# Performance work log

Measured on AMD Instinct MI355X. Metric: run time of the kernel, lower is better.

The kernel has to match this reference:

```python
import jax, jax.numpy as jnp
import numpy as np

H = 16
D = 64
EPS = 1e-6

def _phi(x):
    # elu_feature_map: elu(x) + 1
    return jax.nn.elu(x) + 1.0

def setup_inputs() -> dict:
    key = jax.random.key(0)
    k1, k2, k3, k4 = jax.random.split(key, 4)
    B, N = 4, 4096
    query = jax.random.normal(k1, (B, N, H * D), dtype=jnp.float32)
    key_t = jax.random.normal(k2, (B, N, H * D), dtype=jnp.float32)
    value = jax.random.normal(k3, (B, N, H * D), dtype=jnp.float32)
    W_out = jax.random.normal(k4, (D, H * D), dtype=jnp.float32) * (1.0 / np.sqrt(H * D))
    b_out = jnp.zeros((D,), dtype=jnp.float32)
    return {"query": query, "key": key_t, "value": value, "W_out": W_out, "b_out": b_out}

def reference(query, key, value, W_out, b_out):
    B, N, _ = query.shape
    # b n (h d) -> b h n d
    def split_heads(x):
        return x.reshape(B, N, H, D).transpose(0, 2, 1, 3)
    q = split_heads(query)
    k = split_heads(key)
    v = split_heads(value)
    Q = _phi(q)  # [B,H,N,D]
    K = _phi(k)
    # KV aggregation: O(N D^2)
    KV = jnp.einsum('bhnd,bhnm->bhdm', K, v)          # [B,H,D,D]
    Ksum = K.sum(axis=2)                               # [B,H,D]
    Z = 1.0 / (jnp.einsum('bhnd,bhd->bhn', Q, Ksum) + EPS)  # [B,H,N]
    out = jnp.einsum('bhnd,bhdm,bhn->bhnm', Q, KV, Z)  # [B,H,N,D]
    # b h n d -> b n h d -> (b*n, h*d)
    out = out.transpose(0, 2, 1, 3).reshape(B * N, H * D)
    return out @ W_out.T + b_out
```

## Files before the change

### kernel.cpp

```cpp
#include <hip/hip_runtime.h>

#define B_  4
#define N_  4096
#define H_  16
#define D_  64
#define BH_ 64
#define EPS_ 1e-6f

__device__ __forceinline__ float phi(float x) {
    return x > 0.0f ? x + 1.0f : __expf(x);
}

__global__ __launch_bounds__(256) void k_kvpart(const float* __restrict__ K,
                                                const float* __restrict__ V,
                                                float* __restrict__ kvpart,
                                                float* __restrict__ kspart) {
    const int bh = blockIdx.x;
    const int s  = blockIdx.y;
    const int S  = gridDim.y;
    const int b  = bh >> 4;
    const int h  = bh & 15;
    const int t  = threadIdx.x;

    __shared__ float Ks[64][68];
    __shared__ float Vs[64][68];

    float acc[4][4] = {{0.f}};
    float ksum[4]   = {0.f, 0.f, 0.f, 0.f};
    const int dbase = (t >> 4) * 4;
    const int mbase = (t & 15) * 4;

    const float4* Kf4 = (const float4*)K;
    const float4* Vf4 = (const float4*)V;

    const int rows   = N_ / S;
    const int chunks = rows / 64;

    for (int chunk = 0; chunk < chunks; ++chunk) {
        const int n0 = s * rows + chunk * 64;
        __syncthreads();
#pragma unroll
        for (int rep = 0; rep < 4; ++rep) {
            int idx = t + rep * 256;
            int row = idx >> 4, c4 = idx & 15;
            size_t g = (size_t)(b * N_ + n0 + row) * 256 + h * 16 + c4;
            float4 kv = Kf4[g];
            float4 vv = Vf4[g];
            Ks[row][c4 * 4 + 0] = phi(kv.x);
            Ks[row][c4 * 4 + 1] = phi(kv.y);
            Ks[row][c4 * 4 + 2] = phi(kv.z);
            Ks[row][c4 * 4 + 3] = phi(kv.w);
            *(float4*)&Vs[row][c4 * 4] = vv;
        }
        __syncthreads();
#pragma unroll 8
        for (int n = 0; n < 64; ++n) {
            float4 kd = *(const float4*)&Ks[n][dbase];
            float4 vm = *(const float4*)&Vs[n][mbase];
            float kda[4] = {kd.x, kd.y, kd.z, kd.w};
            float vma[4] = {vm.x, vm.y, vm.z, vm.w};
#pragma unroll
            for (int i = 0; i < 4; ++i) {
#pragma unroll
                for (int j = 0; j < 4; ++j) acc[i][j] += kda[i] * vma[j];
                ksum[i] += kda[i];
            }
        }
    }

    float4* kvp4 = (float4*)kvpart;
    const size_t base = (size_t)(bh * S + s) * 4096;
#pragma unroll
    for (int i = 0; i < 4; ++i) {
        float4 o = make_float4(acc[i][0], acc[i][1], acc[i][2], acc[i][3]);
        kvp4[(base + (size_t)(dbase + i) * 64 + mbase) / 4] = o;
    }
    if ((t & 15) == 0) {
#pragma unroll
        for (int i = 0; i < 4; ++i)
            kspart[(size_t)(bh * S + s) * 64 + dbase + i] = ksum[i];
    }
}

__global__ __launch_bounds__(256) void k_makeM(const float* __restrict__ kvpart,
                                               const float* __restrict__ kspart,
                                               const float* __restrict__ W,
                                               float* __restrict__ M,
                                               float* __restrict__ Ksum,
                                               int S) {
    const int bh = blockIdx.x;
    const int h  = bh & 15;
    const int t  = threadIdx.x;

    __shared__ float KVs[64][68];
    __shared__ float Ws[64][68];

    const float4* kv4 = (const float4*)kvpart;
    const float4* W4  = (const float4*)W;

    for (int idx = t; idx < 1024; idx += 256) {
        int row = idx >> 4, c4 = idx & 15;
        float4 r = make_float4(0.f, 0.f, 0.f, 0.f);
        for (int s = 0; s < S; ++s) {
            float4 a = kv4[(size_t)(bh * S + s) * 1024 + idx];
            r.x += a.x; r.y += a.y; r.z += a.z; r.w += a.w;
        }
        *(float4*)&KVs[row][c4 * 4] = r;
        *(float4*)&Ws[row][c4 * 4] = W4[(size_t)row * 256 + h * 16 + c4];
    }
    if (t < 64) {
        float ks = 0.f;
        for (int s = 0; s < S; ++s) ks += kspart[(size_t)(bh * S + s) * 64 + t];
        Ksum[(size_t)bh * 64 + t] = ks;
    }
    __syncthreads();

    const int dbase = (t >> 4) * 4, jbase = (t & 15) * 4;
    float acc[4][4] = {{0.f}};
#pragma unroll 4
    for (int m4 = 0; m4 < 16; ++m4) {
        float4 kvr[4], wr[4];
#pragma unroll
        for (int i = 0; i < 4; ++i) kvr[i] = *(const float4*)&KVs[dbase + i][m4 * 4];
#pragma unroll
        for (int j = 0; j < 4; ++j) wr[j] = *(const float4*)&Ws[jbase + j][m4 * 4];
#pragma unroll
        for (int i = 0; i < 4; ++i)
#pragma unroll
            for (int j = 0; j < 4; ++j)
                acc[i][j] += kvr[i].x * wr[j].x + kvr[i].y * wr[j].y +
                             kvr[i].z * wr[j].z + kvr[i].w * wr[j].w;
    }
    float4* M4 = (float4*)M;
#pragma unroll
    for (int i = 0; i < 4; ++i)
        M4[((size_t)bh * 4096 + (size_t)(dbase + i) * 64 + jbase) / 4] =
            make_float4(acc[i][0], acc[i][1], acc[i][2], acc[i][3]);
}

__global__ __launch_bounds__(256) void k_out(const float* __restrict__ Q,
                                             const float* __restrict__ M,
                                             const float* __restrict__ Ksum,
                                             float* __restrict__ outpart) {
    const int nc = blockIdx.x;
    const int b  = blockIdx.y;
    const int hs = blockIdx.z;
    const int HS = gridDim.z;
    const int hper = H_ / HS;
    const int n0 = nc * 64;
    const int t  = threadIdx.x;

    __shared__ float Ms[64][68];
    __shared__ float QsT[64][65];
    __shared__ float zp[4][64];
    __shared__ float Kss[64];

    const int ibase = (t >> 4) * 4, jbase = (t & 15) * 4;
    const int qtr = t >> 6, zrow = t & 63;
    float acc[4][4] = {{0.f}};

    const float4* Qf4 = (const float4*)Q;
    const float4* Mf4 = (const float4*)M;

    for (int hh = 0; hh < hper; ++hh) {
        const int h  = hs * hper + hh;
        const int bh = b * 16 + h;
        __syncthreads();
#pragma unroll
        for (int rep = 0; rep < 4; ++rep) {
            int idx = t + rep * 256;
            int row = idx >> 4, c4 = idx & 15;
            *(float4*)&Ms[row][c4 * 4] = Mf4[(size_t)bh * 1024 + idx];
            float4 qq = Qf4[(size_t)(b * N_ + n0 + row) * 256 + h * 16 + c4];
            QsT[c4 * 4 + 0][row] = phi(qq.x);
            QsT[c4 * 4 + 1][row] = phi(qq.y);
            QsT[c4 * 4 + 2][row] = phi(qq.z);
            QsT[c4 * 4 + 3][row] = phi(qq.w);
        }
        if (t < 64) Kss[t] = Ksum[(size_t)bh * 64 + t];
        __syncthreads();

        {
            float part = 0.f;
#pragma unroll
            for (int dd = 0; dd < 16; ++dd) {
                int d = qtr * 16 + dd;
                part += QsT[d][zrow] * Kss[d];
            }
            zp[qtr][zrow] = part;
        }
        __syncthreads();

        float sacc[4][4] = {{0.f}};
#pragma unroll 8
        for (int d = 0; d < 64; ++d) {
            float4 qi = *(const float4*)&QsT[d][ibase];
            float4 mj = *(const float4*)&Ms[d][jbase];
            float qa[4] = {qi.x, qi.y, qi.z, qi.w};
            float ma[4] = {mj.x, mj.y, mj.z, mj.w};
#pragma unroll
            for (int i = 0; i < 4; ++i)
#pragma unroll
                for (int j = 0; j < 4; ++j) sacc[i][j] += qa[i] * ma[j];
        }
#pragma unroll
        for (int i = 0; i < 4; ++i) {
            int r = ibase + i;
            float z = 1.0f / (zp[0][r] + zp[1][r] + zp[2][r] + zp[3][r] + EPS_);
#pragma unroll
            for (int j = 0; j < 4; ++j) acc[i][j] += z * sacc[i][j];
        }
    }

    float4* O4 = (float4*)outpart;
    const size_t slice = (size_t)hs * (B_ * N_ * 64);
#pragma unroll
    for (int i = 0; i < 4; ++i) {
        float4 o = make_float4(acc[i][0], acc[i][1], acc[i][2], acc[i][3]);
        O4[(slice + (size_t)(b * N_ + n0 + ibase + i) * 64 + jbase) / 4] = o;
    }
}

__global__ __launch_bounds__(256) void k_red(const float* __restrict__ outpart,
                                             const float* __restrict__ bout,
                                             float* __restrict__ out, int HS) {
    const int p = blockIdx.x * 256 + threadIdx.x;
    const float4* P4 = (const float4*)outpart;
    const float4* B4 = (const float4*)bout;
    float4 o = B4[p & 15];
    const int stride = B_ * N_ * 64 / 4;
    for (int hs = 0; hs < HS; ++hs) {
        float4 a = P4[(size_t)hs * stride + p];
        o.x += a.x; o.y += a.y; o.z += a.z; o.w += a.w;
    }
    ((float4*)out)[p] = o;
}

extern "C" void kernel_launch(void* const* d_in, const int* in_sizes, int n_in,
                              void* d_out, int out_size, void* d_ws, size_t ws_size,
                              hipStream_t stream) {
    const float* q  = (const float*)d_in[0];
    const float* k  = (const float*)d_in[1];
    const float* v  = (const float*)d_in[2];
    const float* W  = (const float*)d_in[3];
    const float* bo = (const float*)d_in[4];
    float* out = (float*)d_out;

    int S = 16, HS = 4;
    {
        size_t need = ((size_t)BH_ * 16 * 4096 + (size_t)BH_ * 16 * 64 +
                       (size_t)BH_ * 4096 + BH_ * 64 +
                       (size_t)4 * B_ * N_ * 64) * 4;
        if (ws_size < need) { S = 4; HS = 1; }
    }

    float* ws      = (float*)d_ws;
    float* kvpart  = ws;
    float* kspart  = kvpart + (size_t)BH_ * S * 4096;
    float* M       = kspart + (size_t)BH_ * S * 64;
    float* Ksum    = M + (size_t)BH_ * 4096;
    float* outpart = Ksum + (size_t)BH_ * 64;

    k_kvpart<<<dim3(BH_, S), 256, 0, stream>>>(k, v, kvpart, kspart);
    k_makeM<<<BH_, 256, 0, stream>>>(kvpart, kspart, W, M, Ksum, S);
    k_out<<<dim3(N_ / 64, B_, HS), 256, 0, stream>>>(q, M, Ksum, outpart);
    k_red<<<B_ * N_ * 64 / 4 / 256, 256, 0, stream>>>(outpart, bo, out, HS);
}
```

Baseline: 263.5 us.

## Use packed fp16 dot2 in KV and output kernels with larger tiles

Converts phi(K), V, phi(Q), the projected M and Ksum to packed fp16 pairs in shared memory and accumulates with v_dot2 (fp16 inputs, fp32 accumulation). k_kvpart now splits the row chunk across four waves with 8x8 register tiles, then reduces the partials through shared memory. k_out processes 128 rows per block and computes the normaliser inside the main loop, so the separate z pass and its barrier go away. Split counts become compile-time constants and the workspace-size fallback is removed. This costs input precision and raises register pressure.

```diff
diff --git a/kernel.cpp b/kernel.cpp
--- a/kernel.cpp
+++ b/kernel.cpp
@@ -5,10 +5,26 @@
 #define H_  16
 #define D_  64
 #define BH_ 64
+#define S_  8
+#define HS_ 4
 #define EPS_ 1e-6f
+
+typedef _Float16 h2  __attribute__((ext_vector_type(2)));
+typedef float    f4v __attribute__((ext_vector_type(4)));
+
+struct H2x4 { h2 e[4]; };
+
+__device__ __forceinline__ H2x4 ld_h2x4(const h2* p) {
+    f4v r = *(const f4v*)p;
+    return __builtin_bit_cast(H2x4, r);
+}
 
 __device__ __forceinline__ float phi(float x) {
     return x > 0.0f ? x + 1.0f : __expf(x);
+}
+
+__device__ __forceinline__ float fdot2(h2 a, h2 b, float c) {
+    return __builtin_amdgcn_fdot2(a, b, c, false);
 }
 
 __global__ __launch_bounds__(256) void k_kvpart(const float* __restrict__ K,
@@ -17,77 +33,139 @@
                                                 float* __restrict__ kspart) {
     const int bh = blockIdx.x;
     const int s  = blockIdx.y;
-    const int S  = gridDim.y;
     const int b  = bh >> 4;
     const int h  = bh & 15;
     const int t  = threadIdx.x;
-
-    __shared__ float Ks[64][68];
-    __shared__ float Vs[64][68];
-
-    float acc[4][4] = {{0.f}};
-    float ksum[4]   = {0.f, 0.f, 0.f, 0.f};
-    const int dbase = (t >> 4) * 4;
-    const int mbase = (t & 15) * 4;
+    const int w  = t >> 6;
+    const int lane = t & 63;
+
+    __shared__ __align__(16) float pool[2 * 64 * 68];
+    __shared__ float ksred[4][64];
+
+    h2* Kp = (h2*)pool;
+    h2* Vp = (h2*)(pool + 2176);
+
+    const int dbase = (lane >> 3) * 8;
+    const int mbase = (lane & 7) * 8;
+
+    float acc[8][8] = {{0.f}};
+    float ksum[8]   = {0.f};
+    h2 one2; one2.x = (_Float16)1.0f; one2.y = (_Float16)1.0f;
 
     const float4* Kf4 = (const float4*)K;
     const float4* Vf4 = (const float4*)V;
 
-    const int rows   = N_ / S;
-    const int chunks = rows / 64;
-
-    for (int chunk = 0; chunk < chunks; ++chunk) {
-        const int n0 = s * rows + chunk * 64;
+    for (int chunk = 0; chunk < (N_ / S_) / 64; ++chunk) {
+        const int n0 = s * (N_ / S_) + chunk * 64;
         __syncthreads();
 #pragma unroll
-        for (int rep = 0; rep < 4; ++rep) {
+        for (int rep = 0; rep < 2; ++rep) {
             int idx = t + rep * 256;
-            int row = idx >> 4, c4 = idx & 15;
-            size_t g = (size_t)(b * N_ + n0 + row) * 256 + h * 16 + c4;
-            float4 kv = Kf4[g];
-            float4 vv = Vf4[g];
-            Ks[row][c4 * 4 + 0] = phi(kv.x);
-            Ks[row][c4 * 4 + 1] = phi(kv.y);
-            Ks[row][c4 * 4 + 2] = phi(kv.z);
-            Ks[row][c4 * 4 + 3] = phi(kv.w);
-            *(float4*)&Vs[row][c4 * 4] = vv;
+            int rp = idx >> 4, c4 = idx & 15;
+            size_t g = (size_t)(b * N_ + n0 + 2 * rp) * 256 + h * 16 + c4;
+            float4 a = Kf4[g];
+            float4 c = Kf4[g + 256];
+            H2x4 o;
+            o.e[0].x = (_Float16)phi(a.x); o.e[0].y = (_Float16)phi(c.x);
+            o.e[1].x = (_Float16)phi(a.y); o.e[1].y = (_Float16)phi(c.y);
+            o.e[2].x = (_Float16)phi(a.z); o.e[2].y = (_Float16)phi(c.z);
+            o.e[3].x = (_Float16)phi(a.w); o.e[3].y = (_Float16)phi(c.w);
+            *(f4v*)&Kp[rp * 68 + c4 * 4] = __builtin_bit_cast(f4v, o);
+        }
+#pragma unroll
+        for (int rep = 0; rep < 2; ++rep) {
+            int idx = t + rep * 256;
+            int rp = idx >> 4, c4 = idx & 15;
+            size_t g = (size_t)(b * N_ + n0 + 2 * rp) * 256 + h * 16 + c4;
+            float4 a = Vf4[g];
+            float4 c = Vf4[g + 256];
+            H2x4 o;
+            o.e[0].x = (_Float16)a.x; o.e[0].y = (_Float16)c.x;
+            o.e[1].x = (_Float16)a.y; o.e[1].y = (_Float16)c.y;
+            o.e[2].x = (_Float16)a.z; o.e[2].y = (_Float16)c.z;
+            o.e[3].x = (_Float16)a.w; o.e[3].y = (_Float16)c.w;
+            *(f4v*)&Vp[rp * 68 + c4 * 4] = __builtin_bit_cast(f4v, o);
         }
         __syncthreads();
-#pragma unroll 8
-        for (int n = 0; n < 64; ++n) {
-            float4 kd = *(const float4*)&Ks[n][dbase];
-            float4 vm = *(const float4*)&Vs[n][mbase];
-            float kda[4] = {kd.x, kd.y, kd.z, kd.w};
-            float vma[4] = {vm.x, vm.y, vm.z, vm.w};
-#pragma unroll
-            for (int i = 0; i < 4; ++i) {
-#pragma unroll
-                for (int j = 0; j < 4; ++j) acc[i][j] += kda[i] * vma[j];
-                ksum[i] += kda[i];
+#pragma unroll
+        for (int cc = 0; cc < 8; ++cc) {
+            int c = w * 8 + cc;
+            H2x4 kd0 = ld_h2x4(&Kp[c * 68 + dbase]);
+            H2x4 kd1 = ld_h2x4(&Kp[c * 68 + dbase + 4]);
+            H2x4 vm0 = ld_h2x4(&Vp[c * 68 + mbase]);
+            H2x4 vm1 = ld_h2x4(&Vp[c * 68 + mbase + 4]);
+            h2 kd[8] = {kd0.e[0], kd0.e[1], kd0.e[2], kd0.e[3],
+                        kd1.e[0], kd1.e[1], kd1.e[2], kd1.e[3]};
+            h2 vm[8] = {vm0.e[0], vm0.e[1], vm0.e[2], vm0.e[3],
+                        vm1.e[0], vm1.e[1], vm1.e[2], vm1.e[3]};
+#pragma unroll
+            for (int i = 0; i < 8; ++i) {
+#pragma unroll
+                for (int j = 0; j < 8; ++j) acc[i][j] = fdot2(kd[i], vm[j], acc[i][j]);
+                ksum[i] = fdot2(kd[i], one2, ksum[i]);
             }
         }
     }
 
-    float4* kvp4 = (float4*)kvpart;
-    const size_t base = (size_t)(bh * S + s) * 4096;
-#pragma unroll
-    for (int i = 0; i < 4; ++i) {
-        float4 o = make_float4(acc[i][0], acc[i][1], acc[i][2], acc[i][3]);
-        kvp4[(base + (size_t)(dbase + i) * 64 + mbase) / 4] = o;
-    }
-    if ((t & 15) == 0) {
-#pragma unroll
-        for (int i = 0; i < 4; ++i)
-            kspart[(size_t)(bh * S + s) * 64 + dbase + i] = ksum[i];
-    }
+    if ((lane & 7) == 0) {
+#pragma unroll
+        for (int i = 0; i < 8; ++i) ksred[w][dbase + i] = ksum[i];
+    }
+    float* Red = pool;
+    __syncthreads();
+
+#define WRITE_T(slot)                                                          \
+    {   float* T = Red + (slot) * 64 * 68;                                     \
+        _Pragma("unroll")                                                      \
+        for (int i = 0; i < 8; ++i) {                                          \
+            f4v o0 = {acc[i][0], acc[i][1], acc[i][2], acc[i][3]};             \
+            f4v o1 = {acc[i][4], acc[i][5], acc[i][6], acc[i][7]};             \
+            *(f4v*)&T[(dbase + i) * 68 + mbase]     = o0;                      \
+            *(f4v*)&T[(dbase + i) * 68 + mbase + 4] = o1;                      \
+        } }
+#define ADD_T(slot)                                                            \
+    {   float* T = Red + (slot) * 64 * 68;                                     \
+        _Pragma("unroll")                                                      \
+        for (int i = 0; i < 8; ++i) {                                          \
+            f4v r0 = *(f4v*)&T[(dbase + i) * 68 + mbase];                      \
+            f4v r1 = *(f4v*)&T[(dbase + i) * 68 + mbase + 4];                  \
+            acc[i][0] += r0[0]; acc[i][1] += r0[1];                            \
+            acc[i][2] += r0[2]; acc[i][3] += r0[3];                            \
+            acc[i][4] += r1[0]; acc[i][5] += r1[1];                            \
+            acc[i][6] += r1[2]; acc[i][7] += r1[3];                            \
+        } }
+
+    if (w == 1) WRITE_T(0);
+    if (w == 3) WRITE_T(1);
+    __syncthreads();
+    if (w == 0) ADD_T(0);
+    if (w == 2) ADD_T(1);
+    __syncthreads();
+    if (w == 2) WRITE_T(0);
+    __syncthreads();
+    if (w == 0) {
+        ADD_T(0);
+        float4* kvp4 = (float4*)kvpart;
+        const size_t base = (size_t)(bh * S_ + s) * 4096;
+#pragma unroll
+        for (int i = 0; i < 8; ++i) {
+            float4 o0 = make_float4(acc[i][0], acc[i][1], acc[i][2], acc[i][3]);
+            float4 o1 = make_float4(acc[i][4], acc[i][5], acc[i][6], acc[i][7]);
+            kvp4[(base + (size_t)(dbase + i) * 64 + mbase) / 4]     = o0;
+            kvp4[(base + (size_t)(dbase + i) * 64 + mbase + 4) / 4] = o1;
+        }
+        float ks = ksred[0][lane] + ksred[1][lane] + ksred[2][lane] + ksred[3][lane];
+        kspart[(size_t)(bh * S_ + s) * 64 + lane] = ks;
+    }
+#undef WRITE_T
+#undef ADD_T
 }
 
 __global__ __launch_bounds__(256) void k_makeM(const float* __restrict__ kvpart,
                                                const float* __restrict__ kspart,
                                                const float* __restrict__ W,
-                                               float* __restrict__ M,
-                                               float* __restrict__ Ksum,
-                                               int S) {
+                                               float* __restrict__ Mh,
+                                               float* __restrict__ Ksum) {
     const int bh = blockIdx.x;
     const int h  = bh & 15;
     const int t  = threadIdx.x;
@@ -101,8 +179,8 @@
     for (int idx = t; idx < 1024; idx += 256) {
         int row = idx >> 4, c4 = idx & 15;
         float4 r = make_float4(0.f, 0.f, 0.f, 0.f);
-        for (int s = 0; s < S; ++s) {
-            float4 a = kv4[(size_t)(bh * S + s) * 1024 + idx];
+        for (int s = 0; s < S_; ++s) {
+            float4 a = kv4[(size_t)(bh * S_ + s) * 1024 + idx];
             r.x += a.x; r.y += a.y; r.z += a.z; r.w += a.w;
         }
         *(float4*)&KVs[row][c4 * 4] = r;
@@ -110,7 +188,7 @@
     }
     if (t < 64) {
         float ks = 0.f;
-        for (int s = 0; s < S; ++s) ks += kspart[(size_t)(bh * S + s) * 64 + t];
+        for (int s = 0; s < S_; ++s) ks += kspart[(size_t)(bh * S_ + s) * 64 + t];
         Ksum[(size_t)bh * 64 + t] = ks;
     }
     __syncthreads();
@@ -131,105 +209,112 @@
                 acc[i][j] += kvr[i].x * wr[j].x + kvr[i].y * wr[j].y +
                              kvr[i].z * wr[j].z + kvr[i].w * wr[j].w;
     }
-    float4* M4 = (float4*)M;
-#pragma unroll
-    for (int i = 0; i < 4; ++i)
-        M4[((size_t)bh * 4096 + (size_t)(dbase + i) * 64 + jbase) / 4] =
-            make_float4(acc[i][0], acc[i][1], acc[i][2], acc[i][3]);
+    f4v* M4 = (f4v*)Mh;
+#pragma unroll
+    for (int p = 0; p < 2; ++p) {
+        int c = (dbase >> 1) + p;
+        H2x4 o;
+#pragma unroll
+        for (int j = 0; j < 4; ++j) {
+            o.e[j].x = (_Float16)acc[2 * p][j];
+            o.e[j].y = (_Float16)acc[2 * p + 1][j];
+        }
+        M4[((size_t)bh * 2048 + c * 64 + jbase) / 4] = __builtin_bit_cast(f4v, o);
+    }
 }
 
 __global__ __launch_bounds__(256) void k_out(const float* __restrict__ Q,
-                                             const float* __restrict__ M,
+                                             const float* __restrict__ Mh,
                                              const float* __restrict__ Ksum,
                                              float* __restrict__ outpart) {
     const int nc = blockIdx.x;
     const int b  = blockIdx.y;
     const int hs = blockIdx.z;
-    const int HS = gridDim.z;
-    const int hper = H_ / HS;
-    const int n0 = nc * 64;
+    const int n0 = nc * 128;
     const int t  = threadIdx.x;
 
-    __shared__ float Ms[64][68];
-    __shared__ float QsT[64][65];
-    __shared__ float zp[4][64];
-    __shared__ float Kss[64];
-
-    const int ibase = (t >> 4) * 4, jbase = (t & 15) * 4;
-    const int qtr = t >> 6, zrow = t & 63;
-    float acc[4][4] = {{0.f}};
+    __shared__ __align__(16) h2 QpT[32][132];
+    __shared__ __align__(16) h2 Msp[32][68];
+    __shared__ h2 Kssh[32];
+
+    const int ibase = (t >> 4) * 8;
+    const int jbase = (t & 15) * 4;
+    float acc_out[8][4] = {{0.f}};
 
     const float4* Qf4 = (const float4*)Q;
-    const float4* Mf4 = (const float4*)M;
-
-    for (int hh = 0; hh < hper; ++hh) {
-        const int h  = hs * hper + hh;
+    const f4v*    M4  = (const f4v*)Mh;
+
+    for (int hh = 0; hh < 4; ++hh) {
+        const int h  = hs * 4 + hh;
         const int bh = b * 16 + h;
         __syncthreads();
 #pragma unroll
-        for (int rep = 0; rep < 4; ++rep) {
+        for (int rep = 0; rep < 8; ++rep) {
             int idx = t + rep * 256;
             int row = idx >> 4, c4 = idx & 15;
-            *(float4*)&Ms[row][c4 * 4] = Mf4[(size_t)bh * 1024 + idx];
             float4 qq = Qf4[(size_t)(b * N_ + n0 + row) * 256 + h * 16 + c4];
-            QsT[c4 * 4 + 0][row] = phi(qq.x);
-            QsT[c4 * 4 + 1][row] = phi(qq.y);
-            QsT[c4 * 4 + 2][row] = phi(qq.z);
-            QsT[c4 * 4 + 3][row] = phi(qq.w);
-        }
-        if (t < 64) Kss[t] = Ksum[(size_t)bh * 64 + t];
+            h2 p0; p0.x = (_Float16)phi(qq.x); p0.y = (_Float16)phi(qq.y);
+            h2 p1; p1.x = (_Float16)phi(qq.z); p1.y = (_Float16)phi(qq.w);
+            QpT[2 * c4][row]     = p0;
+            QpT[2 * c4 + 1][row] = p1;
+        }
+#pragma unroll
+        for (int rep = 0; rep < 2; ++rep) {
+            int i2 = t + rep * 256;
+            int c = i2 >> 4, j4 = (i2 & 15) * 4;
+            *(f4v*)&Msp[c][j4] = M4[(size_t)bh * 512 + i2];
+        }
+        if (t < 32) {
+            h2 ks; ks.x = (_Float16)Ksum[(size_t)bh * 64 + 2 * t];
+            ks.y = (_Float16)Ksum[(size_t)bh * 64 + 2 * t + 1];
+            Kssh[t] = ks;
+        }
         __syncthreads();
 
-        {
-            float part = 0.f;
-#pragma unroll
-            for (int dd = 0; dd < 16; ++dd) {
-                int d = qtr * 16 + dd;
-                part += QsT[d][zrow] * Kss[d];
+        float sacc[8][4] = {{0.f}};
+        float zacc[8]    = {0.f};
+#pragma unroll 4
+        for (int c = 0; c < 32; ++c) {
+            H2x4 qa = ld_h2x4(&QpT[c][ibase]);
+            H2x4 qb = ld_h2x4(&QpT[c][ibase + 4]);
+            H2x4 mm = ld_h2x4(&Msp[c][jbase]);
+            h2 ks = Kssh[c];
+            h2 q[8] = {qa.e[0], qa.e[1], qa.e[2], qa.e[3],
+                       qb.e[0], qb.e[1], qb.e[2], qb.e[3]};
+#pragma unroll
+            for (int i = 0; i < 8; ++i) {
+                zacc[i] = fdot2(q[i], ks, zacc[i]);
+#pragma unroll
+                for (int j = 0; j < 4; ++j) sacc[i][j] = fdot2(q[i], mm.e[j], sacc[i][j]);
             }
-            zp[qtr][zrow] = part;
-        }
-        __syncthreads();
-
-        float sacc[4][4] = {{0.f}};
-#pragma unroll 8
-        for (int d = 0; d < 64; ++d) {
-            float4 qi = *(const float4*)&QsT[d][ibase];
-            float4 mj = *(const float4*)&Ms[d][jbase];
-            float qa[4] = {qi.x, qi.y, qi.z, qi.w};
-            float ma[4] = {mj.x, mj.y, mj.z, mj.w};
-#pragma unroll
-            for (int i = 0; i < 4; ++i)
-#pragma unroll
-                for (int j = 0; j < 4; ++j) sacc[i][j] += qa[i] * ma[j];
-        }
-#pragma unroll
-        for (int i = 0; i < 4; ++i) {
-            int r = ibase + i;
-            float z = 1.0f / (zp[0][r] + zp[1][r] + zp[2][r] + zp[3][r] + EPS_);
-#pragma unroll
-            for (int j = 0; j < 4; ++j) acc[i][j] += z * sacc[i][j];
+        }
+#pragma unroll
+        for (int i = 0; i < 8; ++i) {
+            float z = 1.0f / (zacc[i] + EPS_);
+#pragma unroll
+            for (int j = 0; j < 4; ++j) acc_out[i][j] += z * sacc[i][j];
         }
     }
 
     float4* O4 = (float4*)outpart;
     const size_t slice = (size_t)hs * (B_ * N_ * 64);
 #pragma unroll
-    for (int i = 0; i < 4; ++i) {
-        float4 o = make_float4(acc[i][0], acc[i][1], acc[i][2], acc[i][3]);
+    for (int i = 0; i < 8; ++i) {
+        float4 o = make_float4(acc_out[i][0], acc_out[i][1], acc_out[i][2], acc_out[i][3]);
         O4[(slice + (size_t)(b * N_ + n0 + ibase + i) * 64 + jbase) / 4] = o;
     }
 }
 
 __global__ __launch_bounds__(256) void k_red(const float* __restrict__ outpart,
                                              const float* __restrict__ bout,
-                                             float* __restrict__ out, int HS) {
+                                             float* __restrict__ out) {
     const int p = blockIdx.x * 256 + threadIdx.x;
     const float4* P4 = (const float4*)outpart;
     const float4* B4 = (const float4*)bout;
     float4 o = B4[p & 15];
     const int stride = B_ * N_ * 64 / 4;
-    for (int hs = 0; hs < HS; ++hs) {
+#pragma unroll
+    for (int hs = 0; hs < HS_; ++hs) {
         float4 a = P4[(size_t)hs * stride + p];
         o.x += a.x; o.y += a.y; o.z += a.z; o.w += a.w;
     }
@@ -246,23 +331,15 @@
     const float* bo = (const float*)d_in[4];
     float* out = (float*)d_out;
 
-    int S = 16, HS = 4;
-    {
-        size_t need = ((size_t)BH_ * 16 * 4096 + (size_t)BH_ * 16 * 64 +
-                       (size_t)BH_ * 4096 + BH_ * 64 +
-                       (size_t)4 * B_ * N_ * 64) * 4;
-        if (ws_size < need) { S = 4; HS = 1; }
-    }
-
     float* ws      = (float*)d_ws;
     float* kvpart  = ws;
-    float* kspart  = kvpart + (size_t)BH_ * S * 4096;
-    float* M       = kspart + (size_t)BH_ * S * 64;
-    float* Ksum    = M + (size_t)BH_ * 4096;
+    float* kspart  = kvpart + (size_t)BH_ * S_ * 4096;
+    float* Mh      = kspart + (size_t)BH_ * S_ * 64;
+    float* Ksum    = Mh + (size_t)BH_ * 2048;
     float* outpart = Ksum + (size_t)BH_ * 64;
 
-    k_kvpart<<<dim3(BH_, S), 256, 0, stream>>>(k, v, kvpart, kspart);
-    k_makeM<<<BH_, 256, 0, stream>>>(kvpart, kspart, W, M, Ksum, S);
-    k_out<<<dim3(N_ / 64, B_, HS), 256, 0, stream>>>(q, M, Ksum, outpart);
-    k_red<<<B_ * N_ * 64 / 4 / 256, 256, 0, stream>>>(outpart, bo, out, HS);
-}
+    k_kvpart<<<dim3(BH_, S_), 256, 0, stream>>>(k, v, kvpart, kspart);
+    k_makeM<<<BH_, 256, 0, stream>>>(kvpart, kspart, W, Mh, Ksum);
+    k_out<<<dim3(N_ / 128, B_, HS_), 256, 0, stream>>>(q, Mh, Ksum, outpart);
+    k_red<<<B_ * N_ * 64 / 4 / 256, 256, 0, stream>>>(outpart, bo, out);
+}
```

New measurement: 248.4 us. 1.06x faster.
